# Optimization experiments

Hardware: AMD Instinct MI355X
Metric: run time of the kernel (lower is better)

The kernel has to match this reference:

```python
import jax, jax.numpy as jnp
import numpy as np

T, B, D, H = 512, 64, 512, 512


def setup_inputs() -> dict:
    key = jax.random.key(0)
    ks = jax.random.split(key, 7)
    stdv = 1.0 / np.sqrt(H)
    u = lambda k, shape: jax.random.uniform(k, shape, jnp.float32, -stdv, stdv)
    return {
        'x': jax.random.normal(ks[0], (T, B, D), jnp.float32),
        'h0': jax.random.normal(ks[1], (B, H), jnp.float32),
        'c0': jax.random.normal(ks[2], (B, H), jnp.float32),
        'w_ih': u(ks[3], (4 * H, D)),
        'b_ih': u(ks[4], (4 * H,)),
        'w_hh': u(ks[5], (4 * H, H)),
        'b_hh': u(ks[6], (4 * H,)),
    }


def reference(x, h0, c0, w_ih, b_ih, w_hh, b_hh):
    # One LSTM layer, forward direction, no dropout, no PackedSequence.
    # gates = Linear_ih(x_t) + Linear_hh(h_{t-1}); split into i,f,g,o along features.
    def step(carry, x_t):
        h, c = carry
        gates = x_t @ w_ih.T + b_ih + h @ w_hh.T + b_hh  # [B, 4H]
        i_g, f_g, g_g, o_g = jnp.split(gates, 4, axis=1)
        c_t = jax.nn.sigmoid(f_g) * c + jax.nn.sigmoid(i_g) * jnp.tanh(g_g)
        h_t = jax.nn.sigmoid(o_g) * jnp.tanh(c_t)
        return (h_t, c_t), h_t

    (h_last, c_last), h_all = jax.lax.scan(step, (h0, c0), x)
    # output [T, B, H], final states [B, H]
    return h_all, h_last, c_last
```

## Files before the change

kernel.cpp:

```cpp
#include <hip/hip_runtime.h>
#include <stdint.h>

#define T_STEPS 512
#define BATCH   64
#define DIM     512
#define NGROUP  8
#define WG_PER_GROUP 32
#define GB      8
#define TBH     (T_STEPS*BATCH*DIM)
#define BH      (BATCH*DIM)
#define TAGM    0x00010001u

typedef __attribute__((ext_vector_type(8))) short short8;
typedef __attribute__((ext_vector_type(4))) float f32x4;
typedef __attribute__((ext_vector_type(4))) unsigned int u32x4;
typedef unsigned short u16;

__device__ __forceinline__ u16 f2bf(float f) {
  union { float f; uint32_t u; } c; c.f = f;
  uint32_t u = c.u;
  return (u16)((u + 0x7FFFu + ((u >> 16) & 1u)) >> 16);
}

__device__ __forceinline__ float fsigmoid(float x) {
  float e = __expf(-x);
  return __builtin_amdgcn_rcpf(1.f + e);
}
__device__ __forceinline__ float ftanh(float x) {
  float e = __expf(2.f * x);
  return 1.f - 2.f * __builtin_amdgcn_rcpf(e + 1.f);
}

__global__ void pack_w_kernel(const float* __restrict__ w_ih,
                              const float* __restrict__ w_hh,
                              uint4* __restrict__ wpack) {
  int j = blockIdx.x;
  for (int u = threadIdx.x; u < 8192; u += 256) {
    int w    = u >> 11;
    int kt   = (u >> 6) & 31;
    int lane = u & 63;
    int n  = w * 512 + j * 16 + (lane & 15);
    int k0 = kt * 32 + 8 * (lane >> 4);
    const float* src = (k0 < 512) ? (w_ih + (size_t)n * 512 + k0)
                                  : (w_hh + (size_t)n * 512 + (k0 - 512));
    uint32_t p0 = f2bf(src[0]) | ((uint32_t)f2bf(src[1]) << 16);
    uint32_t p1 = f2bf(src[2]) | ((uint32_t)f2bf(src[3]) << 16);
    uint32_t p2 = f2bf(src[4]) | ((uint32_t)f2bf(src[5]) << 16);
    uint32_t p3 = f2bf(src[6]) | ((uint32_t)f2bf(src[7]) << 16);
    wpack[(size_t)j * 8192 + u] = make_uint4(p0, p1, p2, p3);
  }
}

__global__ void pack_x_kernel(const float* __restrict__ x, uint4* __restrict__ xbf) {
  size_t i = (size_t)blockIdx.x * 256 + threadIdx.x;
  const float4* src = (const float4*)x + i * 2;
  float4 a = src[0], b = src[1];
  uint32_t p0 = f2bf(a.x) | ((uint32_t)f2bf(a.y) << 16);
  uint32_t p1 = f2bf(a.z) | ((uint32_t)f2bf(a.w) << 16);
  uint32_t p2 = f2bf(b.x) | ((uint32_t)f2bf(b.y) << 16);
  uint32_t p3 = f2bf(b.z) | ((uint32_t)f2bf(b.w) << 16);
  xbf[i] = make_uint4(p0, p1, p2, p3);
}

__launch_bounds__(256, 1)
__global__ void lstm_persist(const float* __restrict__ h0, const float* __restrict__ c0,
                             const float* __restrict__ b_ih, const float* __restrict__ b_hh,
                             const uint4* __restrict__ wpack, const u16* __restrict__ xbf,
                             u16* __restrict__ h_buf, float* __restrict__ out) {
  __shared__ uint4 w_lds[8192];
  __shared__ float c_lds[4][16][16];

  const int tid  = threadIdx.x;
  const int lane = tid & 63;
  const int wv   = tid >> 6;
  const int wg   = blockIdx.x;
  const int grp  = wg & 7;
  const int wgj  = wg >> 3;
  const int B0   = grp * GB;

  for (int i = tid; i < 8192; i += 256) w_lds[i] = wpack[(size_t)wgj * 8192 + i];

  const int pb   = tid >> 4;
  const int pc   = tid & 15;
  const int colg = wgj * 16 + pc;
  const int pbs  = pb & 7;
  float c_reg = c0[(B0 + pbs) * DIM + colg];
  const float bias0 = b_ih[0*512 + colg] + b_hh[0*512 + colg];
  const float bias1 = b_ih[1*512 + colg] + b_hh[1*512 + colg];
  const float bias2 = b_ih[2*512 + colg] + b_hh[2*512 + colg];
  const float bias3 = b_ih[3*512 + colg] + b_hh[3*512 + colg];

  const int m  = lane & 15;
  const int m8 = lane & 7;
  const int kq = 8 * (lane >> 4);

  const short8* wl = (const short8*)w_lds;
  bool sticky = false;

  __syncthreads();

  {
    float h0f = h0[(B0 + pbs) * DIM + colg];
    float h0n = __shfl_xor(h0f, 1);
    if (pb < GB && !(pc & 1)) {
      uint32_t both = (uint32_t)f2bf(h0f) | ((uint32_t)f2bf(h0n) << 16);
      uint32_t v = (both & ~TAGM) | TAGM;
      uint32_t* p = (uint32_t*)(h_buf + ((size_t)(0 * NGROUP + grp) * GB + pb) * DIM + colg);
      __hip_atomic_store(p, v, __ATOMIC_RELAXED, __HIP_MEMORY_SCOPE_AGENT);
    }
  }

  f32x4 xacc;
  {
    f32x4 a0 = (f32x4){0.f,0.f,0.f,0.f}, a1 = (f32x4){0.f,0.f,0.f,0.f};
    const u16* xrow = xbf + (size_t)(0 * BATCH + B0 + m8) * DIM;
    for (int kt = 0; kt < 16; kt += 2) {
      short8 a = *((const short8*)(xrow + kt * 32 + kq));
      a0 = __builtin_amdgcn_mfma_f32_16x16x32_bf16(a, wl[(wv*32+kt)*64+lane], a0, 0,0,0);
      short8 a2 = *((const short8*)(xrow + (kt+1) * 32 + kq));
      a1 = __builtin_amdgcn_mfma_f32_16x16x32_bf16(a2, wl[(wv*32+kt+1)*64+lane], a1, 0,0,0);
    }
    xacc = a0 + a1;
  }

  for (int t = 0; t < T_STEPS; ++t) {
    const int pr = t & 1;
    const u16* tb = h_buf + (size_t)(pr * NGROUP + grp) * GB * DIM;
    const uint32_t e = 1u ^ (((uint32_t)t >> 1) & 1u);
    const int esc = (t < 2) ? 256 : 48;

    union HU { u32x4 u; short8 s; } hq[16];
    {
      uint64_t pa2 = (uint64_t)tb + (uint64_t)(m8 * 1024 + (lane >> 4) * 16);
      int spins = 0;
      for (;;) {
#define HLOADS(FLAGS)                                                          \
  do {                                                                         \
    asm volatile("global_load_dwordx4 %0, %1, off offset:0 "   FLAGS : "=v"(hq[0].u)  : "v"(pa2) : "memory"); \
    asm volatile("global_load_dwordx4 %0, %1, off offset:64 "  FLAGS : "=v"(hq[1].u)  : "v"(pa2) : "memory"); \
    asm volatile("global_load_dwordx4 %0, %1, off offset:128 " FLAGS : "=v"(hq[2].u)  : "v"(pa2) : "memory"); \
    asm volatile("global_load_dwordx4 %0, %1, off offset:192 " FLAGS : "=v"(hq[3].u)  : "v"(pa2) : "memory"); \
    asm volatile("global_load_dwordx4 %0, %1, off offset:256 " FLAGS : "=v"(hq[4].u)  : "v"(pa2) : "memory"); \
    asm volatile("global_load_dwordx4 %0, %1, off offset:320 " FLAGS : "=v"(hq[5].u)  : "v"(pa2) : "memory"); \
    asm volatile("global_load_dwordx4 %0, %1, off offset:384 " FLAGS : "=v"(hq[6].u)  : "v"(pa2) : "memory"); \
    asm volatile("global_load_dwordx4 %0, %1, off offset:448 " FLAGS : "=v"(hq[7].u)  : "v"(pa2) : "memory"); \
    asm volatile("global_load_dwordx4 %0, %1, off offset:512 " FLAGS : "=v"(hq[8].u)  : "v"(pa2) : "memory"); \
    asm volatile("global_load_dwordx4 %0, %1, off offset:576 " FLAGS : "=v"(hq[9].u)  : "v"(pa2) : "memory"); \
    asm volatile("global_load_dwordx4 %0, %1, off offset:640 " FLAGS : "=v"(hq[10].u) : "v"(pa2) : "memory"); \
    asm volatile("global_load_dwordx4 %0, %1, off offset:704 " FLAGS : "=v"(hq[11].u) : "v"(pa2) : "memory"); \
    asm volatile("global_load_dwordx4 %0, %1, off offset:768 " FLAGS : "=v"(hq[12].u) : "v"(pa2) : "memory"); \
    asm volatile("global_load_dwordx4 %0, %1, off offset:832 " FLAGS : "=v"(hq[13].u) : "v"(pa2) : "memory"); \
    asm volatile("global_load_dwordx4 %0, %1, off offset:896 " FLAGS : "=v"(hq[14].u) : "v"(pa2) : "memory"); \
    asm volatile("global_load_dwordx4 %0, %1, off offset:960 " FLAGS : "=v"(hq[15].u) : "v"(pa2) : "memory"); \
  } while (0)
        if (!sticky) HLOADS("sc0");
        else         HLOADS("sc0 sc1");
#undef HLOADS
        asm volatile("s_waitcnt vmcnt(0)" ::: "memory");
        __builtin_amdgcn_sched_barrier(0);
        uint32_t andv = 0xFFFFFFFFu, orv = 0u;
        #pragma unroll
        for (int i = 0; i < 16; ++i) {
          u32x4 v = hq[i].u;
          andv &= v.x & v.y & v.z & v.w;
          orv  |= v.x | v.y | v.z | v.w;
        }
        uint32_t ok = e ? ((andv & TAGM) == TAGM) : ((orv & TAGM) == 0u);
        if (__ballot(ok != 0u) == ~0ull) break;
        if (++spins == esc) sticky = true;
        if (spins > (1 << 16)) break;
      }
      __builtin_amdgcn_sched_barrier(0);
    }

    f32x4 acc0 = xacc, acc1 = (f32x4){0.f,0.f,0.f,0.f};
    #pragma unroll
    for (int kt = 0; kt < 16; kt += 2) {
      acc0 = __builtin_amdgcn_mfma_f32_16x16x32_bf16(hq[kt].s,   wl[(wv*32+16+kt)*64+lane],   acc0, 0,0,0);
      acc1 = __builtin_amdgcn_mfma_f32_16x16x32_bf16(hq[kt+1].s, wl[(wv*32+16+kt+1)*64+lane], acc1, 0,0,0);
    }
    f32x4 acc = acc0 + acc1;

    {
      int r0 = (lane >> 4) * 4;
      c_lds[wv][r0 + 0][lane & 15] = acc[0];
      c_lds[wv][r0 + 1][lane & 15] = acc[1];
      c_lds[wv][r0 + 2][lane & 15] = acc[2];
      c_lds[wv][r0 + 3][lane & 15] = acc[3];
    }
    __syncthreads();

    float gi = fsigmoid(c_lds[0][pbs][pc] + bias0);
    float gf = fsigmoid(c_lds[1][pbs][pc] + bias1);
    float gg = ftanh  (c_lds[2][pbs][pc] + bias2);
    float go = fsigmoid(c_lds[3][pbs][pc] + bias3);
    c_reg = gf * c_reg + gi * gg;
    float h = go * ftanh(c_reg);

    if (t < T_STEPS - 1) {
      {
        float hn = __shfl_xor(h, 1);
        if (pb < GB && !(pc & 1)) {
          uint32_t both = (uint32_t)f2bf(h) | ((uint32_t)f2bf(hn) << 16);
          const uint32_t tagw = 1u ^ ((((uint32_t)t + 1) >> 1) & 1u);
          uint32_t v = (both & ~TAGM) | (tagw * TAGM);
          uint32_t* p = (uint32_t*)(h_buf + ((size_t)((pr ^ 1) * NGROUP + grp) * GB + pb) * DIM + colg);
          __hip_atomic_store(p, v, __ATOMIC_RELAXED, __HIP_MEMORY_SCOPE_AGENT);
        }
      }
      if (pb < GB) out[((size_t)t * BATCH + B0 + pb) * DIM + colg] = h;
      f32x4 a2_0 = (f32x4){0.f,0.f,0.f,0.f}, a2_1 = (f32x4){0.f,0.f,0.f,0.f};
      const u16* xr = xbf + (size_t)((t + 1) * BATCH + B0 + m8) * DIM;
      for (int kt = 0; kt < 16; kt += 2) {
        short8 a = *((const short8*)(xr + kt * 32 + kq));
        a2_0 = __builtin_amdgcn_mfma_f32_16x16x32_bf16(a, wl[(wv*32+kt)*64+lane], a2_0, 0,0,0);
        short8 a2 = *((const short8*)(xr + (kt+1) * 32 + kq));
        a2_1 = __builtin_amdgcn_mfma_f32_16x16x32_bf16(a2, wl[(wv*32+kt+1)*64+lane], a2_1, 0,0,0);
      }
      xacc = a2_0 + a2_1;
    } else if (pb < GB) {
      out[((size_t)t * BATCH + B0 + pb) * DIM + colg] = h;
      out[TBH + (B0 + pb) * DIM + colg]      = h;
      out[TBH + BH + (B0 + pb) * DIM + colg] = c_reg;
    }
  }
}

extern "C" void kernel_launch(void* const* d_in, const int* in_sizes, int n_in,
                              void* d_out, int out_size, void* d_ws, size_t ws_size,
                              hipStream_t stream) {
  (void)in_sizes; (void)n_in; (void)out_size; (void)ws_size;
  const float* x    = (const float*)d_in[0];
  const float* h0   = (const float*)d_in[1];
  const float* c0   = (const float*)d_in[2];
  const float* w_ih = (const float*)d_in[3];
  const float* b_ih = (const float*)d_in[4];
  const float* w_hh = (const float*)d_in[5];
  const float* b_hh = (const float*)d_in[6];
  float* out = (float*)d_out;

  char* ws = (char*)d_ws;
  uint4* wpack = (uint4*)ws;
  u16*   xbf   = (u16*)(ws + ((size_t)4 << 20));
  u16*   hbuf  = (u16*)(ws + ((size_t)36 << 20));

  pack_w_kernel<<<dim3(32),   dim3(256), 0, stream>>>(w_ih, w_hh, wpack);
  pack_x_kernel<<<dim3(8192), dim3(256), 0, stream>>>(x, (uint4*)xbf);

  void* args[] = {(void*)&h0, (void*)&c0, (void*)&b_ih, (void*)&b_hh,
                  (void*)&wpack, (void*)&xbf, (void*)&hbuf, (void*)&out};
  hipError_t e = hipLaunchCooperativeKernel((void*)lstm_persist, dim3(NGROUP * WG_PER_GROUP),
                                            dim3(256), args, 0, stream);
  if (e != hipSuccess) {
    lstm_persist<<<dim3(NGROUP * WG_PER_GROUP), dim3(256), 0, stream>>>(
        h0, c0, b_ih, b_hh, wpack, xbf, hbuf, out);
  }
}
```

Before: 2.897 ms.

## Poll a small probe before full h loads and mirror h into local and far buffers

Each step's h state is now written twice: a plain store to a local buffer and a system-coherent (sc0 sc1) store to a separate far buffer. Waiters first spin on one 16-byte probe load per lane covering the whole tile, and issue the sixteen full h loads only once every tag in the probe is ready. After the escalation threshold they switch to polling the far copy with sc0 sc1 loads. The aim is less memory traffic while spinning and a cheaper fast path for the cross-workgroup handoff. In exchange it adds an extra store per step, one extra round trip before the real loads, and depends on the cache-coherence behaviour of the two buffers.

```diff
diff --git a/kernel.cpp b/kernel.cpp
--- a/kernel.cpp
+++ b/kernel.cpp
@@ -66,7 +66,8 @@
 __global__ void lstm_persist(const float* __restrict__ h0, const float* __restrict__ c0,
                              const float* __restrict__ b_ih, const float* __restrict__ b_hh,
                              const uint4* __restrict__ wpack, const u16* __restrict__ xbf,
-                             u16* __restrict__ h_buf, float* __restrict__ out) {
+                             u16* __restrict__ h_loc, u16* __restrict__ h_far,
+                             float* __restrict__ out) {
   __shared__ uint4 w_lds[8192];
   __shared__ float c_lds[4][16][16];
 
@@ -90,12 +91,16 @@
   const float bias2 = b_ih[2*512 + colg] + b_hh[2*512 + colg];
   const float bias3 = b_ih[3*512 + colg] + b_hh[3*512 + colg];
 
-  const int m  = lane & 15;
   const int m8 = lane & 7;
   const int kq = 8 * (lane >> 4);
 
   const short8* wl = (const short8*)w_lds;
   bool sticky = false;
+
+  const uint64_t stByte = ((uint64_t)pb * DIM + colg) * 2;
+  const uint64_t prByte = (uint64_t)(lane & 7) * 1024 +
+                          ((uint64_t)(lane >> 3) + (uint64_t)(lane & 7) * 8) * 16;
+  const uint64_t ldByte = (uint64_t)m8 * 1024 + (uint64_t)(lane >> 4) * 16;
 
   __syncthreads();
 
@@ -105,8 +110,10 @@
     if (pb < GB && !(pc & 1)) {
       uint32_t both = (uint32_t)f2bf(h0f) | ((uint32_t)f2bf(h0n) << 16);
       uint32_t v = (both & ~TAGM) | TAGM;
-      uint32_t* p = (uint32_t*)(h_buf + ((size_t)(0 * NGROUP + grp) * GB + pb) * DIM + colg);
-      __hip_atomic_store(p, v, __ATOMIC_RELAXED, __HIP_MEMORY_SCOPE_AGENT);
+      uint64_t aL = (uint64_t)(h_loc + (size_t)(0 * NGROUP + grp) * GB * DIM) + stByte;
+      uint64_t aF = (uint64_t)(h_far + (size_t)(0 * NGROUP + grp) * GB * DIM) + stByte;
+      asm volatile("global_store_dword %0, %1, off"          :: "v"(aL), "v"(v) : "memory");
+      asm volatile("global_store_dword %0, %1, off sc0 sc1"  :: "v"(aF), "v"(v) : "memory");
     }
   }
 
@@ -125,15 +132,34 @@
 
   for (int t = 0; t < T_STEPS; ++t) {
     const int pr = t & 1;
-    const u16* tb = h_buf + (size_t)(pr * NGROUP + grp) * GB * DIM;
+    const uint64_t tbL = (uint64_t)(h_loc + (size_t)(pr * NGROUP + grp) * GB * DIM);
+    const uint64_t tbF = (uint64_t)(h_far + (size_t)(pr * NGROUP + grp) * GB * DIM);
     const uint32_t e = 1u ^ (((uint32_t)t >> 1) & 1u);
     const int esc = (t < 2) ? 256 : 48;
 
     union HU { u32x4 u; short8 s; } hq[16];
     {
-      uint64_t pa2 = (uint64_t)tb + (uint64_t)(m8 * 1024 + (lane >> 4) * 16);
       int spins = 0;
       for (;;) {
+        const uint64_t tb = sticky ? tbF : tbL;
+        {
+          u32x4 s;
+          uint64_t pa = tb + prByte;
+          if (!sticky) asm volatile("global_load_dwordx4 %0, %1, off sc0"     : "=v"(s) : "v"(pa) : "memory");
+          else         asm volatile("global_load_dwordx4 %0, %1, off sc0 sc1" : "=v"(s) : "v"(pa) : "memory");
+          asm volatile("s_waitcnt vmcnt(0)" ::: "memory");
+          __builtin_amdgcn_sched_barrier(0);
+          uint32_t andv = s.x & s.y & s.z & s.w;
+          uint32_t orv  = s.x | s.y | s.z | s.w;
+          uint32_t ok = e ? ((andv & TAGM) == TAGM) : ((orv & TAGM) == 0u);
+          if (__ballot(ok != 0u) != ~0ull) {
+            if (++spins == esc) sticky = true;
+            if (spins > (1 << 16)) break;
+            continue;
+          }
+        }
+        {
+          uint64_t pa2 = tb + ldByte;
 #define HLOADS(FLAGS)                                                          \
   do {                                                                         \
     asm volatile("global_load_dwordx4 %0, %1, off offset:0 "   FLAGS : "=v"(hq[0].u)  : "v"(pa2) : "memory"); \
@@ -153,22 +179,23 @@
     asm volatile("global_load_dwordx4 %0, %1, off offset:896 " FLAGS : "=v"(hq[14].u) : "v"(pa2) : "memory"); \
     asm volatile("global_load_dwordx4 %0, %1, off offset:960 " FLAGS : "=v"(hq[15].u) : "v"(pa2) : "memory"); \
   } while (0)
-        if (!sticky) HLOADS("sc0");
-        else         HLOADS("sc0 sc1");
+          if (!sticky) HLOADS("sc0");
+          else         HLOADS("sc0 sc1");
 #undef HLOADS
-        asm volatile("s_waitcnt vmcnt(0)" ::: "memory");
-        __builtin_amdgcn_sched_barrier(0);
-        uint32_t andv = 0xFFFFFFFFu, orv = 0u;
-        #pragma unroll
-        for (int i = 0; i < 16; ++i) {
-          u32x4 v = hq[i].u;
-          andv &= v.x & v.y & v.z & v.w;
-          orv  |= v.x | v.y | v.z | v.w;
+          asm volatile("s_waitcnt vmcnt(0)" ::: "memory");
+          __builtin_amdgcn_sched_barrier(0);
+          uint32_t andv = 0xFFFFFFFFu, orv = 0u;
+          #pragma unroll
+          for (int i = 0; i < 16; ++i) {
+            u32x4 v = hq[i].u;
+            andv &= v.x & v.y & v.z & v.w;
+            orv  |= v.x | v.y | v.z | v.w;
+          }
+          uint32_t ok = e ? ((andv & TAGM) == TAGM) : ((orv & TAGM) == 0u);
+          if (__ballot(ok != 0u) == ~0ull) break;
+          if (++spins == esc) sticky = true;
+          if (spins > (1 << 16)) break;
         }
-        uint32_t ok = e ? ((andv & TAGM) == TAGM) : ((orv & TAGM) == 0u);
-        if (__ballot(ok != 0u) == ~0ull) break;
-        if (++spins == esc) sticky = true;
-        if (spins > (1 << 16)) break;
       }
       __builtin_amdgcn_sched_barrier(0);
     }
@@ -204,8 +231,10 @@
           uint32_t both = (uint32_t)f2bf(h) | ((uint32_t)f2bf(hn) << 16);
           const uint32_t tagw = 1u ^ ((((uint32_t)t + 1) >> 1) & 1u);
           uint32_t v = (both & ~TAGM) | (tagw * TAGM);
-          uint32_t* p = (uint32_t*)(h_buf + ((size_t)((pr ^ 1) * NGROUP + grp) * GB + pb) * DIM + colg);
-          __hip_atomic_store(p, v, __ATOMIC_RELAXED, __HIP_MEMORY_SCOPE_AGENT);
+          uint64_t aL = (uint64_t)(h_loc + (size_t)((pr ^ 1) * NGROUP + grp) * GB * DIM) + stByte;
+          uint64_t aF = (uint64_t)(h_far + (size_t)((pr ^ 1) * NGROUP + grp) * GB * DIM) + stByte;
+          asm volatile("global_store_dword %0, %1, off"         :: "v"(aL), "v"(v) : "memory");
+          asm volatile("global_store_dword %0, %1, off sc0 sc1" :: "v"(aF), "v"(v) : "memory");
         }
       }
       if (pb < GB) out[((size_t)t * BATCH + B0 + pb) * DIM + colg] = h;
@@ -242,17 +271,18 @@
   char* ws = (char*)d_ws;
   uint4* wpack = (uint4*)ws;
   u16*   xbf   = (u16*)(ws + ((size_t)4 << 20));
-  u16*   hbuf  = (u16*)(ws + ((size_t)36 << 20));
+  u16*   hloc  = (u16*)(ws + ((size_t)36 << 20));
+  u16*   hfar  = (u16*)(ws + ((size_t)37 << 20));
 
   pack_w_kernel<<<dim3(32),   dim3(256), 0, stream>>>(w_ih, w_hh, wpack);
   pack_x_kernel<<<dim3(8192), dim3(256), 0, stream>>>(x, (uint4*)xbf);
 
   void* args[] = {(void*)&h0, (void*)&c0, (void*)&b_ih, (void*)&b_hh,
-                  (void*)&wpack, (void*)&xbf, (void*)&hbuf, (void*)&out};
+                  (void*)&wpack, (void*)&xbf, (void*)&hloc, (void*)&hfar, (void*)&out};
   hipError_t e = hipLaunchCooperativeKernel((void*)lstm_persist, dim3(NGROUP * WG_PER_GROUP),
                                             dim3(256), args, 0, stream);
   if (e != hipSuccess) {
     lstm_persist<<<dim3(NGROUP * WG_PER_GROUP), dim3(256), 0, stream>>>(
-        h0, c0, b_ih, b_hh, wpack, xbf, hbuf, out);
-  }
-}
+        h0, c0, b_ih, b_hh, wpack, xbf, hloc, hfar, out);
+  }
+}
```

New measurement: 2.757 ms. 1.05x faster.
